# Performance work log

Measured on AMD Instinct MI355X. Metric: run time of the kernel, lower is better.

## Reference

```python
import jax, jax.numpy as jnp
import numpy as np

N = 4096
IN_FEATS = 64
HIDDEN = 128
STEPS = 3
SCALE = 3.0
LJ_EPS = 0.1
LJ_SIGMA = 3.5
LJ_MIX = 0.1  # 'auto' branch: pot = exp(-r/scale)*relu(score) + 0.1*lj
LN_EPS = 1e-5


def setup_inputs() -> dict:
    key = jax.random.key(0)
    ks = jax.random.split(key, 12)
    x = jax.random.normal(ks[0], (N, IN_FEATS), dtype=jnp.float32)
    # sparse-ish 0/1 adjacency (float, as multiplied in the torch code)
    adj = (jax.random.uniform(ks[1], (N, N)) < 0.02).astype(jnp.float32)
    # positive pairwise distances in Angstrom-like range
    dist_mat = jax.random.uniform(ks[2], (N, N), dtype=jnp.float32) * 10.0 + 0.5
    s_in = 1.0 / np.sqrt(IN_FEATS)
    s_h = 1.0 / np.sqrt(HIDDEN)
    s_2h = 1.0 / np.sqrt(2 * HIDDEN)
    params = {
        'W_in': jax.random.uniform(ks[3], (IN_FEATS, HIDDEN), minval=-s_in, maxval=s_in),
        'b_in': jnp.zeros((HIDDEN,), jnp.float32),
        'W_msg': jax.random.uniform(ks[4], (HIDDEN, HIDDEN), minval=-s_h, maxval=s_h),
        'b_msg': jnp.zeros((HIDDEN,), jnp.float32),
        'W_u1': jax.random.uniform(ks[5], (2 * HIDDEN, HIDDEN), minval=-s_2h, maxval=s_2h),
        'b_u1': jnp.zeros((HIDDEN,), jnp.float32),
        'W_u2': jax.random.uniform(ks[6], (HIDDEN, HIDDEN), minval=-s_h, maxval=s_h),
        'b_u2': jnp.zeros((HIDDEN,), jnp.float32),
        'gamma': jnp.ones((HIDDEN,), jnp.float32),
        'beta': jnp.zeros((HIDDEN,), jnp.float32),
    }
    return {'x': x, 'adj': adj, 'dist_mat': dist_mat, **params}


def _layernorm(x, gamma, beta):
    mu = jnp.mean(x, axis=-1, keepdims=True)
    var = jnp.mean(jnp.square(x - mu), axis=-1, keepdims=True)
    return (x - mu) * jax.lax.rsqrt(var + LN_EPS) * gamma + beta


def reference(x, adj, dist_mat, W_in, b_in, W_msg, b_msg, W_u1, b_u1, W_u2, b_u2, gamma, beta):
    h = x @ W_in + b_in  # (n, hidden)
    # distance-only terms are loop-invariant
    r_safe = jnp.clip(dist_mat, 1e-6, None)
    sr6 = (LJ_SIGMA / r_safe) ** 6
    lj = 4.0 * LJ_EPS * (sr6 * sr6 - sr6)          # (n, n)
    decay = jnp.exp(-dist_mat / SCALE)             # (n, n)
    pot_const = LJ_MIX * lj                        # 'auto' branch constant part
    for _ in range(STEPS):
        # torch code computes msg_lin(h) but never uses it (dead code) -> skipped
        # pot_scalar[i,j] = <h_i, h_j>, computed without (n,n,d) materialization
        pot_scalar = h @ h.T                       # (n, n)
        pot = decay * jax.nn.relu(pot_scalar) + pot_const
        # m_i = sum_j pot[i,j]*adj[i,j]*h_j == masked-weighted matmul
        m = (pot * adj) @ h                        # (n, hidden)
        concat = jnp.concatenate([h, m], axis=-1)  # (n, 2*hidden)
        delta = jax.nn.relu(concat @ W_u1 + b_u1) @ W_u2 + b_u2
        h = _layernorm(h + delta, gamma, beta)
    return h
```

## Files before the change

kernel.cpp:

```cpp
#include <hip/hip_runtime.h>
#include <hip/hip_bf16.h>

#define NN   4096
#define HID  128
#define INFE 64
#define KE   160
#define RPB  4

typedef unsigned short u16;
typedef unsigned int   u32;

__device__ __forceinline__ float bflo(u32 w){ return __uint_as_float(w << 16); }
__device__ __forceinline__ float bfhi(u32 w){ return __uint_as_float(w & 0xffff0000u); }
__device__ __forceinline__ u16 f2b(float f) { __hip_bfloat16 h = __float2bfloat16(f); return *(u16*)&h; }

__global__ __launch_bounds__(128) void k_h0(
    const float* __restrict__ x, const float* __restrict__ Win, const float* __restrict__ bin,
    float* __restrict__ hdst, u16* __restrict__ bdst)
{
    __shared__ float xl[INFE];
    const int r = blockIdx.x;
    const int d = threadIdx.x;
    if (d < INFE) xl[d] = x[(size_t)r*INFE + d];
    __syncthreads();
    float acc = bin[d];
    #pragma unroll 8
    for (int k = 0; k < INFE; ++k)
        acc = fmaf(xl[k], Win[k*HID + d], acc);
    hdst[(size_t)r*HID + d] = acc;
    bdst[(size_t)r*HID + d] = f2b(acc);
}

__global__ __launch_bounds__(256) void k_build(
    const float* __restrict__ adj, const float* __restrict__ dist,
    float4* __restrict__ edges, int* __restrict__ nnzp)
{
    __shared__ int wtot[4];
    const int r    = blockIdx.x;
    const int t    = threadIdx.x;
    const int w    = t >> 6;
    const int lane = t & 63;
    const float4* arow = (const float4*)(adj + (size_t)r*NN);
    float4 a[4];
    #pragma unroll
    for (int q = 0; q < 4; ++q) a[q] = arow[t + 256*q];
    int cnt = 0;
    #pragma unroll
    for (int q = 0; q < 4; ++q) {
        cnt += (a[q].x != 0.f) + (a[q].y != 0.f) + (a[q].z != 0.f) + (a[q].w != 0.f);
    }
    int incl = cnt;
    #pragma unroll
    for (int off = 1; off < 64; off <<= 1) {
        int v = __shfl_up(incl, off);
        if (lane >= off) incl += v;
    }
    if (lane == 63) wtot[w] = incl;
    __syncthreads();
    int wbase = 0;
    #pragma unroll
    for (int i = 0; i < 4; ++i) if (i < w) wbase += wtot[i];
    const int total = wtot[0] + wtot[1] + wtot[2] + wtot[3];
    int slot = wbase + (incl - cnt);
    float4* erow = edges + (size_t)r*KE;
    const float* drow = dist + (size_t)r*NN;
    #pragma unroll
    for (int q = 0; q < 4; ++q) {
        float v[4] = {a[q].x, a[q].y, a[q].z, a[q].w};
        #pragma unroll
        for (int u = 0; u < 4; ++u) {
            if (v[u] != 0.f) {
                if (slot < KE) {
                    int c = 4*(t + 256*q) + u;
                    float d  = fmaxf(drow[c], 1e-6f);
                    float dw1 = v[u] * __expf(-d * (1.0f/3.0f));
                    float tt = 3.5f / d, t2 = tt*tt, t6 = t2*t2*t2;
                    float dw2 = v[u] * 0.04f * (t6*t6 - t6);
                    erow[slot] = make_float4(__int_as_float(c), dw1, dw2, 0.f);
                }
                ++slot;
            }
        }
    }
    const int n  = total < KE ? total : KE;
    const int np = (n + 15) / 16 * 16;
    for (int i = n + t; i < np; i += 256)
        erow[i] = make_float4(__int_as_float(0), 0.f, 0.f, 0.f);
    if (t == 0) nnzp[r] = np;
}

__global__ __launch_bounds__(256) void k_fstep(
    const float4* __restrict__ edges, const int* __restrict__ nnzp,
    const float* __restrict__ h, const u16* __restrict__ hb,
    const float* __restrict__ Wu1, const float* __restrict__ bu1,
    const float* __restrict__ Wu2, const float* __restrict__ bu2,
    const float* __restrict__ gam, const float* __restrict__ bet,
    float* __restrict__ hout, u16* __restrict__ bout)
{
    __shared__ __align__(16) float4 eds[RPB][KE];
    __shared__ int npl[RPB];
    __shared__ __align__(16) float hs[RPB][HID];
    __shared__ __align__(16) float ms[RPB][HID];
    __shared__ __align__(16) float h1s[RPB][HID];
    __shared__ float hn[RPB][HID];
    const int t    = threadIdx.x;
    const int w    = t >> 6;
    const int lane = t & 63;
    const int g    = lane >> 5;
    const int j    = lane & 31;
    const int r0   = blockIdx.x * RPB;
    const int r    = r0 + w;

    if (t < RPB) npl[t] = nnzp[r0 + t];
    const float4 hi4 = *(const float4*)(h + (size_t)r*HID + 4*j);
    if (g == 0) *(float4*)&hs[w][4*j] = hi4;
    __syncthreads();
    #pragma unroll
    for (int rr = 0; rr < RPB; ++rr) {
        const float4* er = edges + (size_t)(r0+rr)*KE;
        for (int i = t; i < npl[rr]; i += 256) eds[rr][i] = er[i];
    }
    __syncthreads();

    const int np = npl[w];
    float4 macc = make_float4(0.f, 0.f, 0.f, 0.f);
    for (int e0 = 0; e0 < np; e0 += 16) {
        float4 ed[8]; uint2 hj16[8]; float p[8];
        #pragma unroll
        for (int q = 0; q < 8; ++q) ed[q] = eds[w][e0 + g + 2*q];
        #pragma unroll
        for (int q = 0; q < 8; ++q) {
            int c = __float_as_int(ed[q].x);
            hj16[q] = *(const uint2*)(hb + (size_t)c*HID + 4*j);
        }
        float4 hjf[8];
        #pragma unroll
        for (int q = 0; q < 8; ++q) {
            hjf[q].x = bflo(hj16[q].x); hjf[q].y = bfhi(hj16[q].x);
            hjf[q].z = bflo(hj16[q].y); hjf[q].w = bfhi(hj16[q].y);
            p[q] = hi4.x*hjf[q].x;
            p[q] = fmaf(hi4.y, hjf[q].y, p[q]);
            p[q] = fmaf(hi4.z, hjf[q].z, p[q]);
            p[q] = fmaf(hi4.w, hjf[q].w, p[q]);
        }
        #pragma unroll
        for (int mask = 1; mask <= 16; mask <<= 1) {
            #pragma unroll
            for (int q = 0; q < 8; ++q) p[q] += __shfl_xor(p[q], mask);
        }
        #pragma unroll
        for (int q = 0; q < 8; ++q) {
            float wq = fmaf(ed[q].y, fmaxf(p[q], 0.f), ed[q].z);
            macc.x = fmaf(wq, hjf[q].x, macc.x);
            macc.y = fmaf(wq, hjf[q].y, macc.y);
            macc.z = fmaf(wq, hjf[q].z, macc.z);
            macc.w = fmaf(wq, hjf[q].w, macc.w);
        }
    }
    macc.x += __shfl_xor(macc.x, 32);
    macc.y += __shfl_xor(macc.y, 32);
    macc.z += __shfl_xor(macc.z, 32);
    macc.w += __shfl_xor(macc.w, 32);
    if (g == 0) *(float4*)&ms[w][4*j] = macc;
    __syncthreads();

    {
        const int half = t >> 7;
        const int d    = t & 127;
        const int ra = 2*half, rb = ra + 1;
        float bb = bu1[d];
        float a0 = bb, a1 = bb;
        for (int k = 0; k < HID; k += 4) {
            float w0 = Wu1[(k+0)*HID + d], w1 = Wu1[(k+1)*HID + d];
            float w2 = Wu1[(k+2)*HID + d], w3 = Wu1[(k+3)*HID + d];
            float4 caa = *(const float4*)&hs[ra][k];
            float4 cbb = *(const float4*)&hs[rb][k];
            a0 = fmaf(caa.x,w0,a0); a0 = fmaf(caa.y,w1,a0); a0 = fmaf(caa.z,w2,a0); a0 = fmaf(caa.w,w3,a0);
            a1 = fmaf(cbb.x,w0,a1); a1 = fmaf(cbb.y,w1,a1); a1 = fmaf(cbb.z,w2,a1); a1 = fmaf(cbb.w,w3,a1);
        }
        for (int k = 0; k < HID; k += 4) {
            float w0 = Wu1[(HID+k+0)*HID + d], w1 = Wu1[(HID+k+1)*HID + d];
            float w2 = Wu1[(HID+k+2)*HID + d], w3 = Wu1[(HID+k+3)*HID + d];
            float4 caa = *(const float4*)&ms[ra][k];
            float4 cbb = *(const float4*)&ms[rb][k];
            a0 = fmaf(caa.x,w0,a0); a0 = fmaf(caa.y,w1,a0); a0 = fmaf(caa.z,w2,a0); a0 = fmaf(caa.w,w3,a0);
            a1 = fmaf(cbb.x,w0,a1); a1 = fmaf(cbb.y,w1,a1); a1 = fmaf(cbb.z,w2,a1); a1 = fmaf(cbb.w,w3,a1);
        }
        h1s[ra][d] = fmaxf(a0, 0.f);
        h1s[rb][d] = fmaxf(a1, 0.f);
    }
    __syncthreads();
    {
        const int half = t >> 7;
        const int d    = t & 127;
        const int ra = 2*half, rb = ra + 1;
        float bb = bu2[d];
        float b0 = bb, b1 = bb;
        for (int k = 0; k < HID; k += 4) {
            float w0 = Wu2[(k+0)*HID + d], w1 = Wu2[(k+1)*HID + d];
            float w2 = Wu2[(k+2)*HID + d], w3 = Wu2[(k+3)*HID + d];
            float4 caa = *(const float4*)&h1s[ra][k];
            float4 cbb = *(const float4*)&h1s[rb][k];
            b0 = fmaf(caa.x,w0,b0); b0 = fmaf(caa.y,w1,b0); b0 = fmaf(caa.z,w2,b0); b0 = fmaf(caa.w,w3,b0);
            b1 = fmaf(cbb.x,w0,b1); b1 = fmaf(cbb.y,w1,b1); b1 = fmaf(cbb.z,w2,b1); b1 = fmaf(cbb.w,w3,b1);
        }
        hn[ra][d] = hs[ra][d] + b0;
        hn[rb][d] = hs[rb][d] + b1;
    }
    __syncthreads();
    {
        float v0 = hn[w][lane], v1 = hn[w][lane + 64];
        float s = v0 + v1;
        #pragma unroll
        for (int mask = 1; mask <= 32; mask <<= 1) s += __shfl_xor(s, mask);
        float mu = s * (1.0f/128.0f);
        float z0 = v0 - mu, z1 = v1 - mu;
        float vv = fmaf(z0, z0, z1*z1);
        #pragma unroll
        for (int mask = 1; mask <= 32; mask <<= 1) vv += __shfl_xor(vv, mask);
        float rstd = rsqrtf(vv * (1.0f/128.0f) + 1e-5f);
        float o0 = fmaf(z0 * rstd, gam[lane],      bet[lane]);
        float o1 = fmaf(z1 * rstd, gam[lane + 64], bet[lane + 64]);
        hout[(size_t)r*HID + lane]      = o0;
        hout[(size_t)r*HID + lane + 64] = o1;
        bout[(size_t)r*HID + lane]      = f2b(o0);
        bout[(size_t)r*HID + lane + 64] = f2b(o1);
    }
}

extern "C" void kernel_launch(void* const* d_in, const int* in_sizes, int n_in,
                              void* d_out, int out_size, void* d_ws, size_t ws_size,
                              hipStream_t stream)
{
    const float* x    = (const float*)d_in[0];
    const float* adj  = (const float*)d_in[1];
    const float* dist = (const float*)d_in[2];
    const float* Win  = (const float*)d_in[3];
    const float* bin  = (const float*)d_in[4];
    const float* Wu1  = (const float*)d_in[7];
    const float* bu1  = (const float*)d_in[8];
    const float* Wu2  = (const float*)d_in[9];
    const float* bu2  = (const float*)d_in[10];
    const float* gam  = (const float*)d_in[11];
    const float* bet  = (const float*)d_in[12];

    const size_t ebytes = (size_t)NN * KE * sizeof(float4);
    const size_t cbytes = ((size_t)NN * sizeof(int) + 255) & ~255;
    const size_t hb32   = (size_t)NN * HID * sizeof(float);
    const size_t hb16   = (size_t)NN * HID * sizeof(u16);
    const size_t need   = ebytes + cbytes + hb32 + 2*hb16;

    if (ws_size >= need) {
        char* p = (char*)d_ws;
        float4* edges = (float4*)p;            p += ebytes;
        int*    nnzp  = (int*)p;               p += cbytes;
        float*  hA    = (float*)p;             p += hb32;
        u16*    bA    = (u16*)p;               p += hb16;
        u16*    bB    = (u16*)p;               p += hb16;
        float*  hB    = (float*)d_out;

        k_build<<<NN, 256, 0, stream>>>(adj, dist, edges, nnzp);
        k_h0<<<NN, 128, 0, stream>>>(x, Win, bin, hA, bA);
        k_fstep<<<NN/RPB, 256, 0, stream>>>(edges, nnzp, hA, bA, Wu1, bu1, Wu2, bu2, gam, bet, hB, bB);
        k_fstep<<<NN/RPB, 256, 0, stream>>>(edges, nnzp, hB, bB, Wu1, bu1, Wu2, bu2, gam, bet, hA, bA);
        k_fstep<<<NN/RPB, 256, 0, stream>>>(edges, nnzp, hA, bA, Wu1, bu1, Wu2, bu2, gam, bet, hB, bB);
    } else {
        if (ws_size >= ebytes + cbytes + hb32 + 2*hb16) {  }
        if (ws_size >= ebytes + cbytes + hb32 + hb16) {
            char* p = (char*)d_ws;
            float4* edges = (float4*)p;        p += ebytes;
            int*    nnzp  = (int*)p;           p += cbytes;
            float*  hA    = (float*)p;         p += hb32;
            u16*    bA    = (u16*)p;
            float*  hB    = (float*)d_out;
            u16*    bB    = (u16*)((char*)d_out + hb32) - (hb16/sizeof(u16));
            k_build<<<NN, 256, 0, stream>>>(adj, dist, edges, nnzp);
            k_h0<<<NN, 128, 0, stream>>>(x, Win, bin, hA, bA);
            k_fstep<<<NN/RPB, 256, 0, stream>>>(edges, nnzp, hA, bA, Wu1, bu1, Wu2, bu2, gam, bet, hB, bB);
            k_fstep<<<NN/RPB, 256, 0, stream>>>(edges, nnzp, hB, bB, Wu1, bu1, Wu2, bu2, gam, bet, hA, bA);
            k_fstep<<<NN/RPB, 256, 0, stream>>>(edges, nnzp, hA, bA, Wu1, bu1, Wu2, bu2, gam, bet, hB, bB);
        }
    }
}
```

Before: 271.1 us.

## Split edge build into adjacency compaction and parallel per-edge weight kernel

Replaces the single per-row build kernel with a compaction kernel that handles four rows per block and stores only column index and adjacency value. A second flat-parallel kernel then gathers the distance values and computes the decay and LJ weights for each edge. The aim is more memory-level parallelism on the adjacency stream and removal of divergent scattered distance loads from the scan kernel. The cost is an extra launch and an intermediate buffer round trip. The workspace-size fallback path is also dropped.

```diff
diff --git a/kernel.cpp b/kernel.cpp
--- a/kernel.cpp
+++ b/kernel.cpp
@@ -31,62 +31,87 @@
     bdst[(size_t)r*HID + d] = f2b(acc);
 }
 
-__global__ __launch_bounds__(256) void k_build(
-    const float* __restrict__ adj, const float* __restrict__ dist,
-    float4* __restrict__ edges, int* __restrict__ nnzp)
-{
-    __shared__ int wtot[4];
-    const int r    = blockIdx.x;
+__global__ __launch_bounds__(256) void k_compact(
+    const float* __restrict__ adj, int2* __restrict__ cols, int* __restrict__ nnzp)
+{
+    __shared__ int wtot[RPB][4];
+    const int r0   = blockIdx.x * RPB;
     const int t    = threadIdx.x;
     const int w    = t >> 6;
     const int lane = t & 63;
-    const float4* arow = (const float4*)(adj + (size_t)r*NN);
-    float4 a[4];
-    #pragma unroll
-    for (int q = 0; q < 4; ++q) a[q] = arow[t + 256*q];
-    int cnt = 0;
-    #pragma unroll
-    for (int q = 0; q < 4; ++q) {
-        cnt += (a[q].x != 0.f) + (a[q].y != 0.f) + (a[q].z != 0.f) + (a[q].w != 0.f);
-    }
-    int incl = cnt;
+    float4 a[RPB][4];
+    #pragma unroll
+    for (int rr = 0; rr < RPB; ++rr) {
+        const float4* arow = (const float4*)(adj + (size_t)(r0+rr)*NN);
+        #pragma unroll
+        for (int q = 0; q < 4; ++q) a[rr][q] = arow[t + 256*q];
+    }
+    int cnt[RPB], incl[RPB];
+    #pragma unroll
+    for (int rr = 0; rr < RPB; ++rr) {
+        int c = 0;
+        #pragma unroll
+        for (int q = 0; q < 4; ++q)
+            c += (a[rr][q].x != 0.f) + (a[rr][q].y != 0.f) + (a[rr][q].z != 0.f) + (a[rr][q].w != 0.f);
+        cnt[rr] = c; incl[rr] = c;
+    }
     #pragma unroll
     for (int off = 1; off < 64; off <<= 1) {
-        int v = __shfl_up(incl, off);
-        if (lane >= off) incl += v;
-    }
-    if (lane == 63) wtot[w] = incl;
-    __syncthreads();
-    int wbase = 0;
-    #pragma unroll
-    for (int i = 0; i < 4; ++i) if (i < w) wbase += wtot[i];
-    const int total = wtot[0] + wtot[1] + wtot[2] + wtot[3];
-    int slot = wbase + (incl - cnt);
-    float4* erow = edges + (size_t)r*KE;
-    const float* drow = dist + (size_t)r*NN;
-    #pragma unroll
-    for (int q = 0; q < 4; ++q) {
-        float v[4] = {a[q].x, a[q].y, a[q].z, a[q].w};
-        #pragma unroll
-        for (int u = 0; u < 4; ++u) {
-            if (v[u] != 0.f) {
-                if (slot < KE) {
-                    int c = 4*(t + 256*q) + u;
-                    float d  = fmaxf(drow[c], 1e-6f);
-                    float dw1 = v[u] * __expf(-d * (1.0f/3.0f));
-                    float tt = 3.5f / d, t2 = tt*tt, t6 = t2*t2*t2;
-                    float dw2 = v[u] * 0.04f * (t6*t6 - t6);
-                    erow[slot] = make_float4(__int_as_float(c), dw1, dw2, 0.f);
+        int v0 = __shfl_up(incl[0], off);
+        int v1 = __shfl_up(incl[1], off);
+        int v2 = __shfl_up(incl[2], off);
+        int v3 = __shfl_up(incl[3], off);
+        if (lane >= off) { incl[0]+=v0; incl[1]+=v1; incl[2]+=v2; incl[3]+=v3; }
+    }
+    if (lane == 63) {
+        #pragma unroll
+        for (int rr = 0; rr < RPB; ++rr) wtot[rr][w] = incl[rr];
+    }
+    __syncthreads();
+    #pragma unroll
+    for (int rr = 0; rr < RPB; ++rr) {
+        int wbase = 0;
+        #pragma unroll
+        for (int i = 0; i < 4; ++i) if (i < w) wbase += wtot[rr][i];
+        const int total = wtot[rr][0] + wtot[rr][1] + wtot[rr][2] + wtot[rr][3];
+        int slot = wbase + (incl[rr] - cnt[rr]);
+        int2* crow = cols + (size_t)(r0+rr)*KE;
+        #pragma unroll
+        for (int q = 0; q < 4; ++q) {
+            float v[4] = {a[rr][q].x, a[rr][q].y, a[rr][q].z, a[rr][q].w};
+            #pragma unroll
+            for (int u = 0; u < 4; ++u) {
+                if (v[u] != 0.f) {
+                    if (slot < KE)
+                        crow[slot] = make_int2(4*(t + 256*q) + u, __float_as_int(v[u]));
+                    ++slot;
                 }
-                ++slot;
             }
         }
-    }
-    const int n  = total < KE ? total : KE;
-    const int np = (n + 15) / 16 * 16;
-    for (int i = n + t; i < np; i += 256)
-        erow[i] = make_float4(__int_as_float(0), 0.f, 0.f, 0.f);
-    if (t == 0) nnzp[r] = np;
+        const int n  = total < KE ? total : KE;
+        const int np = (n + 15) / 16 * 16;
+        for (int i = n + t; i < np; i += 256)
+            crow[i] = make_int2(0, 0);
+        if (t == 0) nnzp[r0+rr] = np;
+    }
+}
+
+__global__ __launch_bounds__(256) void k_weight(
+    const int2* __restrict__ cols, const int* __restrict__ nnzp,
+    const float* __restrict__ dist, float4* __restrict__ edges)
+{
+    const int tid = blockIdx.x*256 + threadIdx.x;
+    const int r   = tid / KE;
+    const int i   = tid - r*KE;
+    if (i >= nnzp[r]) return;
+    int2 ca = cols[(size_t)r*KE + i];
+    int   c = ca.x;
+    float a = __int_as_float(ca.y);
+    float d  = fmaxf(dist[(size_t)r*NN + c], 1e-6f);
+    float dw1 = a * __expf(-d * (1.0f/3.0f));
+    float tt = 3.5f / d, t2 = tt*tt, t6 = t2*t2*t2;
+    float dw2 = a * 0.04f * (t6*t6 - t6);
+    edges[(size_t)r*KE + i] = make_float4(__int_as_float(c), dw1, dw2, 0.f);
 }
 
 __global__ __launch_bounds__(256) void k_fstep(
@@ -245,40 +270,24 @@
     const float* bet  = (const float*)d_in[12];
 
     const size_t ebytes = (size_t)NN * KE * sizeof(float4);
+    const size_t lbytes = (size_t)NN * KE * sizeof(int2);
     const size_t cbytes = ((size_t)NN * sizeof(int) + 255) & ~255;
     const size_t hb32   = (size_t)NN * HID * sizeof(float);
     const size_t hb16   = (size_t)NN * HID * sizeof(u16);
-    const size_t need   = ebytes + cbytes + hb32 + 2*hb16;
-
-    if (ws_size >= need) {
-        char* p = (char*)d_ws;
-        float4* edges = (float4*)p;            p += ebytes;
-        int*    nnzp  = (int*)p;               p += cbytes;
-        float*  hA    = (float*)p;             p += hb32;
-        u16*    bA    = (u16*)p;               p += hb16;
-        u16*    bB    = (u16*)p;               p += hb16;
-        float*  hB    = (float*)d_out;
-
-        k_build<<<NN, 256, 0, stream>>>(adj, dist, edges, nnzp);
-        k_h0<<<NN, 128, 0, stream>>>(x, Win, bin, hA, bA);
-        k_fstep<<<NN/RPB, 256, 0, stream>>>(edges, nnzp, hA, bA, Wu1, bu1, Wu2, bu2, gam, bet, hB, bB);
-        k_fstep<<<NN/RPB, 256, 0, stream>>>(edges, nnzp, hB, bB, Wu1, bu1, Wu2, bu2, gam, bet, hA, bA);
-        k_fstep<<<NN/RPB, 256, 0, stream>>>(edges, nnzp, hA, bA, Wu1, bu1, Wu2, bu2, gam, bet, hB, bB);
-    } else {
-        if (ws_size >= ebytes + cbytes + hb32 + 2*hb16) {  }
-        if (ws_size >= ebytes + cbytes + hb32 + hb16) {
-            char* p = (char*)d_ws;
-            float4* edges = (float4*)p;        p += ebytes;
-            int*    nnzp  = (int*)p;           p += cbytes;
-            float*  hA    = (float*)p;         p += hb32;
-            u16*    bA    = (u16*)p;
-            float*  hB    = (float*)d_out;
-            u16*    bB    = (u16*)((char*)d_out + hb32) - (hb16/sizeof(u16));
-            k_build<<<NN, 256, 0, stream>>>(adj, dist, edges, nnzp);
-            k_h0<<<NN, 128, 0, stream>>>(x, Win, bin, hA, bA);
-            k_fstep<<<NN/RPB, 256, 0, stream>>>(edges, nnzp, hA, bA, Wu1, bu1, Wu2, bu2, gam, bet, hB, bB);
-            k_fstep<<<NN/RPB, 256, 0, stream>>>(edges, nnzp, hB, bB, Wu1, bu1, Wu2, bu2, gam, bet, hA, bA);
-            k_fstep<<<NN/RPB, 256, 0, stream>>>(edges, nnzp, hA, bA, Wu1, bu1, Wu2, bu2, gam, bet, hB, bB);
-        }
-    }
-}
+
+    char* p = (char*)d_ws;
+    float4* edges = (float4*)p;            p += ebytes;
+    int2*   cols  = (int2*)p;              p += lbytes;
+    int*    nnzp  = (int*)p;               p += cbytes;
+    float*  hA    = (float*)p;             p += hb32;
+    u16*    bA    = (u16*)p;               p += hb16;
+    u16*    bB    = (u16*)p;               p += hb16;
+    float*  hB    = (float*)d_out;
+
+    k_compact<<<NN/RPB, 256, 0, stream>>>(adj, cols, nnzp);
+    k_weight<<<NN*KE/256, 256, 0, stream>>>(cols, nnzp, dist, edges);
+    k_h0<<<NN, 128, 0, stream>>>(x, Win, bin, hA, bA);
+    k_fstep<<<NN/RPB, 256, 0, stream>>>(edges, nnzp, hA, bA, Wu1, bu1, Wu2, bu2, gam, bet, hB, bB);
+    k_fstep<<<NN/RPB, 256, 0, stream>>>(edges, nnzp, hB, bB, Wu1, bu1, Wu2, bu2, gam, bet, hA, bA);
+    k_fstep<<<NN/RPB, 256, 0, stream>>>(edges, nnzp, hA, bA, Wu1, bu1, Wu2, bu2, gam, bet, hB, bB);
+}
```

After: 271.8 us. No clear change (+0.2%).

## Compact adjacency with shared atomics, two rows per block, coalesced edge writes

Applied to the files above, without the earlier changes.

The edge-build kernel now handles two adjacency rows per block. Nonzero columns are gathered into shared memory through an LDS atomic counter instead of a wave scan plus cross-wave prefix. Distances are then fetched and edge records written in a dense per-thread loop rather than from divergent per-lane branches. Edge order within a row now depends on atomic timing, which changes the summation order downstream. Truncation at KE now keeps an arbitrary subset rather than the first KE columns. The host wrapper drops the fallback workspace path.

```diff
diff --git a/kernel.cpp b/kernel.cpp
--- a/kernel.cpp
+++ b/kernel.cpp
@@ -35,58 +35,56 @@
     const float* __restrict__ adj, const float* __restrict__ dist,
     float4* __restrict__ edges, int* __restrict__ nnzp)
 {
-    __shared__ int wtot[4];
-    const int r    = blockIdx.x;
-    const int t    = threadIdx.x;
-    const int w    = t >> 6;
-    const int lane = t & 63;
-    const float4* arow = (const float4*)(adj + (size_t)r*NN);
-    float4 a[4];
-    #pragma unroll
-    for (int q = 0; q < 4; ++q) a[q] = arow[t + 256*q];
-    int cnt = 0;
-    #pragma unroll
-    for (int q = 0; q < 4; ++q) {
-        cnt += (a[q].x != 0.f) + (a[q].y != 0.f) + (a[q].z != 0.f) + (a[q].w != 0.f);
-    }
-    int incl = cnt;
-    #pragma unroll
-    for (int off = 1; off < 64; off <<= 1) {
-        int v = __shfl_up(incl, off);
-        if (lane >= off) incl += v;
-    }
-    if (lane == 63) wtot[w] = incl;
-    __syncthreads();
-    int wbase = 0;
-    #pragma unroll
-    for (int i = 0; i < 4; ++i) if (i < w) wbase += wtot[i];
-    const int total = wtot[0] + wtot[1] + wtot[2] + wtot[3];
-    int slot = wbase + (incl - cnt);
-    float4* erow = edges + (size_t)r*KE;
-    const float* drow = dist + (size_t)r*NN;
-    #pragma unroll
-    for (int q = 0; q < 4; ++q) {
-        float v[4] = {a[q].x, a[q].y, a[q].z, a[q].w};
-        #pragma unroll
-        for (int u = 0; u < 4; ++u) {
-            if (v[u] != 0.f) {
-                if (slot < KE) {
-                    int c = 4*(t + 256*q) + u;
-                    float d  = fmaxf(drow[c], 1e-6f);
-                    float dw1 = v[u] * __expf(-d * (1.0f/3.0f));
-                    float tt = 3.5f / d, t2 = tt*tt, t6 = t2*t2*t2;
-                    float dw2 = v[u] * 0.04f * (t6*t6 - t6);
-                    erow[slot] = make_float4(__int_as_float(c), dw1, dw2, 0.f);
+    __shared__ int cnt[2];
+    __shared__ int   cl[2][KE];
+    __shared__ float ca[2][KE];
+    const int r0 = blockIdx.x * 2;
+    const int t  = threadIdx.x;
+    if (t < 2) cnt[t] = 0;
+    __syncthreads();
+    float4 av[2][4];
+    #pragma unroll
+    for (int rr = 0; rr < 2; ++rr) {
+        const float4* arow = (const float4*)(adj + (size_t)(r0+rr)*NN);
+        #pragma unroll
+        for (int q = 0; q < 4; ++q) av[rr][q] = arow[t + 256*q];
+    }
+    #pragma unroll
+    for (int rr = 0; rr < 2; ++rr) {
+        #pragma unroll
+        for (int q = 0; q < 4; ++q) {
+            float a4[4] = {av[rr][q].x, av[rr][q].y, av[rr][q].z, av[rr][q].w};
+            if (a4[0] != 0.f || a4[1] != 0.f || a4[2] != 0.f || a4[3] != 0.f) {
+                #pragma unroll
+                for (int u = 0; u < 4; ++u) {
+                    if (a4[u] != 0.f) {
+                        int pos = atomicAdd(&cnt[rr], 1);
+                        if (pos < KE) { cl[rr][pos] = 4*(t + 256*q) + u; ca[rr][pos] = a4[u]; }
+                    }
                 }
-                ++slot;
             }
         }
     }
-    const int n  = total < KE ? total : KE;
-    const int np = (n + 15) / 16 * 16;
-    for (int i = n + t; i < np; i += 256)
-        erow[i] = make_float4(__int_as_float(0), 0.f, 0.f, 0.f);
-    if (t == 0) nnzp[r] = np;
+    __syncthreads();
+    #pragma unroll
+    for (int rr = 0; rr < 2; ++rr) {
+        const int n  = cnt[rr] < KE ? cnt[rr] : KE;
+        const int np = (n + 15) / 16 * 16;
+        float4* erow = edges + (size_t)(r0+rr)*KE;
+        for (int i = n + t; i < np; i += 256)
+            erow[i] = make_float4(__int_as_float(0), 0.f, 0.f, 0.f);
+        const float* drow = dist + (size_t)(r0+rr)*NN;
+        for (int i = t; i < n; i += 256) {
+            int   c = cl[rr][i];
+            float a = ca[rr][i];
+            float d  = fmaxf(drow[c], 1e-6f);
+            float dw1 = a * __expf(-d * (1.0f/3.0f));
+            float tt = 3.5f / d, t2 = tt*tt, t6 = t2*t2*t2;
+            float dw2 = a * 0.04f * (t6*t6 - t6);
+            erow[i] = make_float4(__int_as_float(c), dw1, dw2, 0.f);
+        }
+        if (t == 0) nnzp[r0+rr] = np;
+    }
 }
 
 __global__ __launch_bounds__(256) void k_fstep(
@@ -248,37 +246,18 @@
     const size_t cbytes = ((size_t)NN * sizeof(int) + 255) & ~255;
     const size_t hb32   = (size_t)NN * HID * sizeof(float);
     const size_t hb16   = (size_t)NN * HID * sizeof(u16);
-    const size_t need   = ebytes + cbytes + hb32 + 2*hb16;
-
-    if (ws_size >= need) {
-        char* p = (char*)d_ws;
-        float4* edges = (float4*)p;            p += ebytes;
-        int*    nnzp  = (int*)p;               p += cbytes;
-        float*  hA    = (float*)p;             p += hb32;
-        u16*    bA    = (u16*)p;               p += hb16;
-        u16*    bB    = (u16*)p;               p += hb16;
-        float*  hB    = (float*)d_out;
-
-        k_build<<<NN, 256, 0, stream>>>(adj, dist, edges, nnzp);
-        k_h0<<<NN, 128, 0, stream>>>(x, Win, bin, hA, bA);
-        k_fstep<<<NN/RPB, 256, 0, stream>>>(edges, nnzp, hA, bA, Wu1, bu1, Wu2, bu2, gam, bet, hB, bB);
-        k_fstep<<<NN/RPB, 256, 0, stream>>>(edges, nnzp, hB, bB, Wu1, bu1, Wu2, bu2, gam, bet, hA, bA);
-        k_fstep<<<NN/RPB, 256, 0, stream>>>(edges, nnzp, hA, bA, Wu1, bu1, Wu2, bu2, gam, bet, hB, bB);
-    } else {
-        if (ws_size >= ebytes + cbytes + hb32 + 2*hb16) {  }
-        if (ws_size >= ebytes + cbytes + hb32 + hb16) {
-            char* p = (char*)d_ws;
-            float4* edges = (float4*)p;        p += ebytes;
-            int*    nnzp  = (int*)p;           p += cbytes;
-            float*  hA    = (float*)p;         p += hb32;
-            u16*    bA    = (u16*)p;
-            float*  hB    = (float*)d_out;
-            u16*    bB    = (u16*)((char*)d_out + hb32) - (hb16/sizeof(u16));
-            k_build<<<NN, 256, 0, stream>>>(adj, dist, edges, nnzp);
-            k_h0<<<NN, 128, 0, stream>>>(x, Win, bin, hA, bA);
-            k_fstep<<<NN/RPB, 256, 0, stream>>>(edges, nnzp, hA, bA, Wu1, bu1, Wu2, bu2, gam, bet, hB, bB);
-            k_fstep<<<NN/RPB, 256, 0, stream>>>(edges, nnzp, hB, bB, Wu1, bu1, Wu2, bu2, gam, bet, hA, bA);
-            k_fstep<<<NN/RPB, 256, 0, stream>>>(edges, nnzp, hA, bA, Wu1, bu1, Wu2, bu2, gam, bet, hB, bB);
-        }
-    }
-}
+
+    char* p = (char*)d_ws;
+    float4* edges = (float4*)p;            p += ebytes;
+    int*    nnzp  = (int*)p;               p += cbytes;
+    float*  hA    = (float*)p;             p += hb32;
+    u16*    bA    = (u16*)p;               p += hb16;
+    u16*    bB    = (u16*)p;               p += hb16;
+    float*  hB    = (float*)d_out;
+
+    k_build<<<NN/2, 256, 0, stream>>>(adj, dist, edges, nnzp);
+    k_h0<<<NN, 128, 0, stream>>>(x, Win, bin, hA, bA);
+    k_fstep<<<NN/RPB, 256, 0, stream>>>(edges, nnzp, hA, bA, Wu1, bu1, Wu2, bu2, gam, bet, hB, bB);
+    k_fstep<<<NN/RPB, 256, 0, stream>>>(edges, nnzp, hB, bB, Wu1, bu1, Wu2, bu2, gam, bet, hA, bA);
+    k_fstep<<<NN/RPB, 256, 0, stream>>>(edges, nnzp, hA, bA, Wu1, bu1, Wu2, bu2, gam, bet, hB, bB);
+}
```

Result: faster. 264.8 us (-2.3%).
